# Performance work log

Measured on AMD Instinct MI355X. Metric: run time of the kernel, lower is better.

Reference implementation:

```python
import jax, jax.numpy as jnp
import numpy as np

B, N, H, NB, NCT = 8, 4096, 1024, 128, 33
LN_EPS = 1e-5


def setup_inputs() -> dict:
    key = jax.random.key(0)
    ks = jax.random.split(key, 12)
    x = jax.random.normal(ks[0], (B, N, H), dtype=jnp.float32)
    cancer_type = jax.random.randint(ks[1], (B,), 0, NCT)
    block_ids = jax.random.randint(ks[2], (B, N), 0, NB)
    pad_mask = jnp.zeros((B, N), dtype=bool)
    s1 = 1.0 / np.sqrt(H)
    s2 = 1.0 / np.sqrt(H // 2)
    return {
        "x": x,
        "cancer_type": cancer_type,
        "block_ids": block_ids,
        "pad_mask": pad_mask,
        "W1": jax.random.normal(ks[3], (H, H // 2), jnp.float32) * s1,
        "b1": jnp.zeros((H // 2,), jnp.float32),
        "W2": jax.random.normal(ks[4], (H // 2, 1), jnp.float32) * s2,
        "b2": jnp.zeros((1,), jnp.float32),
        "ct_emb": jax.random.normal(ks[5], (NCT, NB), jnp.float32) * 0.1,
        "Wp": jax.random.normal(ks[6], (H, H), jnp.float32) * s1,
        "bp": jnp.zeros((H,), jnp.float32),
        "ln_g": jnp.ones((H,), jnp.float32),
        "ln_b": jnp.zeros((H,), jnp.float32),
    }


def reference(x, cancer_type, block_ids, pad_mask, W1, b1, W2, b2, ct_emb, Wp, bp, ln_g, ln_b):
    nb = ct_emb.shape[1]
    # gate MLP: (B,N)
    h = jnp.tanh(x @ W1 + b1)
    gate = (h @ W2 + b2)[..., 0]
    valid = ~pad_mask
    # block membership mask (B, NB, N)
    mask = (block_ids[:, None, :] == jnp.arange(nb)[None, :, None]) & valid[:, None, :]
    neg_inf = jnp.float32(-jnp.inf)
    scores = jnp.where(mask, gate[:, None, :], neg_inf)
    # stable masked softmax over N; empty blocks -> all-zero weights (nan_to_num(0))
    m = jnp.max(scores, axis=-1, keepdims=True)
    m = jnp.where(jnp.isfinite(m), m, 0.0)
    e = jnp.where(mask, jnp.exp(scores - m), 0.0)
    denom = jnp.sum(e, axis=-1, keepdims=True)
    w = jnp.where(denom > 0, e / jnp.maximum(denom, 1e-30), 0.0)
    # cancer-type modulation: weights * (1 + 0.1*ct_mod[:,bid])
    ct_mod = ct_emb[cancer_type]  # (B, NB)
    w = w * (1.0 + 0.1 * ct_mod)[:, :, None]
    # pooled per-block token (B, NB, H)
    pooled = jnp.einsum('bkn,bnh->bkh', w, x)
    # block_proj: Linear -> LayerNorm -> ELU (dropout = eval identity)
    y = pooled @ Wp + bp
    mu = jnp.mean(y, axis=-1, keepdims=True)
    var = jnp.mean((y - mu) ** 2, axis=-1, keepdims=True)
    y = (y - mu) * jax.lax.rsqrt(var + LN_EPS) * ln_g + ln_b
    y = jax.nn.elu(y)
    has_b = jnp.any(mask, axis=-1)              # (B, NB)
    present = jnp.any(has_b, axis=0)            # (NB,) torch loop skips blocks absent everywhere
    block_tokens = jnp.where(present[None, :, None], y, 0.0)
    return block_tokens, has_b
```

## Files before the change

### kernel.cpp

```cpp
#include <hip/hip_runtime.h>

#define NTOK 4096
#define HDIM 1024
#define HHALF 512
#define NBLK 128
#define CAP 256
#define XELEMS 33554432ull

typedef __attribute__((ext_vector_type(8))) short short8;
typedef __attribute__((ext_vector_type(4))) float f32x4;
typedef short bf16s;

__device__ __forceinline__ short f2bf(float f) {
    unsigned u = __builtin_bit_cast(unsigned, f);
    u = (u + 0x7fffu + ((u >> 16) & 1u)) >> 16;
    return (short)u;
}
__device__ __forceinline__ void gload_lds16(const void* g, void* l) {
    __builtin_amdgcn_global_load_lds(
        (const __attribute__((address_space(1))) unsigned int*)g,
        (__attribute__((address_space(3))) unsigned int*)l, 16, 0, 0);
}
__device__ __forceinline__ float fast_tanh(float v) {
    float e = __expf(2.0f * v);
    return 1.0f - 2.0f / (e + 1.0f);
}

__global__ void k_xcvt(const float* __restrict__ in, bf16s* __restrict__ out) {
    for (size_t i = ((size_t)blockIdx.x * 256 + threadIdx.x) * 8; i < XELEMS;
         i += (size_t)gridDim.x * 256 * 8) {
        float4 a = *reinterpret_cast<const float4*>(&in[i]);
        float4 b = *reinterpret_cast<const float4*>(&in[i + 4]);
        short h[8] = {f2bf(a.x), f2bf(a.y), f2bf(a.z), f2bf(a.w),
                      f2bf(b.x), f2bf(b.y), f2bf(b.z), f2bf(b.w)};
        *reinterpret_cast<int4*>(&out[i]) = *reinterpret_cast<const int4*>(h);
    }
}

__global__ void k_tcvt2(const float* __restrict__ W1, const float* __restrict__ Wp,
                        bf16s* __restrict__ w1t, bf16s* __restrict__ wpt) {
    __shared__ float tile[64][65];
    const int by = blockIdx.y;
    const float* in = (by < 8) ? W1 : Wp;
    bf16s* out = (by < 8) ? w1t : wpt;
    const int Nc = (by < 8) ? HHALF : HDIM;
    const int n0 = ((by < 8) ? by : (by - 8)) * 64;
    const int k0 = blockIdx.x * 64;
    const int tx = threadIdx.x & 63, ty = threadIdx.x >> 6;
    #pragma unroll
    for (int i = 0; i < 16; ++i) {
        int r = ty + i * 4;
        tile[r][tx] = in[(size_t)(k0 + r) * Nc + n0 + tx];
    }
    __syncthreads();
    #pragma unroll
    for (int i = 0; i < 16; ++i) {
        int r = ty + i * 4;
        out[(size_t)(n0 + r) * 1024 + k0 + tx] = f2bf(tile[tx][r]);
    }
}

__global__ __launch_bounds__(512, 1) void k_gemm8(
    const bf16s* __restrict__ xb, const bf16s* __restrict__ w1t,
    const float* __restrict__ b1, const float* __restrict__ w2,
    float* __restrict__ partial)
{
    __shared__ alignas(16) bf16s As[2][256 * 32];
    __shared__ alignas(16) bf16s Bs[2][256 * 32];

    const int tid = threadIdx.x;
    const int lane = tid & 63;
    const int wv = tid >> 6;
    const int wm = wv >> 2;
    const int wn = wv & 3;
    const int phys = blockIdx.x;
    const int logical = (phys & 7) * 32 + (phys >> 3);
    const int row0 = (logical >> 1) * 256;
    const int ct   = logical & 1;
    const int col0 = ct * 256;
    const int c0 = lane & 15, khalf = lane >> 4;

    const int sj = (lane & 3) ^ ((lane >> 3) & 3);
    const int rA0 = ((wv & 4) ? 128 : 0) + (wv & 3) * 16 + (lane >> 2);
    const int rB0 = wv * 16 + (lane >> 2);
    const bf16s* aS0 = &xb [(size_t)(row0 + rA0) * HDIM + sj * 8];
    const bf16s* aS1 = aS0 + (size_t)64 * HDIM;
    const bf16s* bS0 = &w1t[(size_t)(col0 + rB0) * HDIM + sj * 8];
    const bf16s* bS1 = bS0 + (size_t)128 * HDIM;
    const int adst0 = (((wv & 4) ? 128 : 0) + (wv & 3) * 16) * 32 + lane * 8;
    const int adst1 = adst0 + 64 * 32;
    const int bdst0 = (wv * 16) * 32 + lane * 8;
    const int bdst1 = bdst0 + 128 * 32;

    const int ch8 = (khalf ^ ((c0 >> 1) & 3)) * 8;
    const int arA = (wm * 128 + c0) * 32 + ch8;
    const int brB = (wn * 64 + c0) * 32 + ch8;

    f32x4 acc[8][4] = {};
    short8 bvv[4];
    short8 av[4];

#define MFMA16(MB)                                                            \
    __builtin_amdgcn_s_setprio(1);                                           \
    _Pragma("unroll")                                                         \
    for (int n = 0; n < 4; ++n)                                               \
        _Pragma("unroll")                                                     \
        for (int m = 0; m < 4; ++m)                                           \
            acc[(MB) + m][n] =                                                \
                __builtin_amdgcn_mfma_f32_16x16x32_bf16(av[m], bvv[n],        \
                                                        acc[(MB) + m][n], 0, 0, 0); \
    __builtin_amdgcn_s_setprio(0);

    gload_lds16(aS0, &As[0][adst0]);
    gload_lds16(aS1, &As[0][adst1]);
    gload_lds16(bS0, &Bs[0][bdst0]);
    gload_lds16(bS1, &Bs[0][bdst1]);
    gload_lds16(aS0 + 32, &As[1][adst0]);
    gload_lds16(bS0 + 32, &Bs[1][bdst0]);

    for (int it = 0; it < 16; ++it) {
        const int ka = 2 * it, kb = 2 * it + 1;
        const bool nl = (it < 15);

        gload_lds16(aS1 + kb * 32, &As[1][adst1]);
        gload_lds16(bS1 + kb * 32, &Bs[1][bdst1]);
        asm volatile("s_waitcnt vmcnt(4)" ::: "memory");
        __builtin_amdgcn_s_barrier();
        #pragma unroll
        for (int m = 0; m < 4; ++m)
            av[m] = *reinterpret_cast<const short8*>(&As[0][arA + m * 512]);
        #pragma unroll
        for (int n = 0; n < 4; ++n)
            bvv[n] = *reinterpret_cast<const short8*>(&Bs[0][brB + n * 512]);
        asm volatile("s_waitcnt lgkmcnt(0)" ::: "memory");
        __builtin_amdgcn_sched_barrier(0);
        MFMA16(0)
        __builtin_amdgcn_s_barrier();

        #pragma unroll
        for (int m = 0; m < 4; ++m)
            av[m] = *reinterpret_cast<const short8*>(&As[0][arA + (4 + m) * 512]);
        if (nl) {
            gload_lds16(aS0 + (ka + 2) * 32, &As[0][adst0]);
            gload_lds16(bS0 + (ka + 2) * 32, &Bs[0][bdst0]);
        }
        __builtin_amdgcn_s_barrier();
        asm volatile("s_waitcnt lgkmcnt(0)" ::: "memory");
        __builtin_amdgcn_sched_barrier(0);
        MFMA16(4)
        __builtin_amdgcn_s_barrier();

        if (nl) {
            gload_lds16(aS1 + (ka + 2) * 32, &As[0][adst1]);
            gload_lds16(bS1 + (ka + 2) * 32, &Bs[0][bdst1]);
            asm volatile("s_waitcnt vmcnt(4)" ::: "memory");
        } else {
            asm volatile("s_waitcnt vmcnt(0)" ::: "memory");
        }
        __builtin_amdgcn_s_barrier();
        #pragma unroll
        for (int m = 0; m < 4; ++m)
            av[m] = *reinterpret_cast<const short8*>(&As[1][arA + m * 512]);
        #pragma unroll
        for (int n = 0; n < 4; ++n)
            bvv[n] = *reinterpret_cast<const short8*>(&Bs[1][brB + n * 512]);
        asm volatile("s_waitcnt lgkmcnt(0)" ::: "memory");
        __builtin_amdgcn_sched_barrier(0);
        MFMA16(0)
        __builtin_amdgcn_s_barrier();

        #pragma unroll
        for (int m = 0; m < 4; ++m)
            av[m] = *reinterpret_cast<const short8*>(&As[1][arA + (4 + m) * 512]);
        if (nl) {
            gload_lds16(aS0 + (kb + 2) * 32, &As[1][adst0]);
            gload_lds16(bS0 + (kb + 2) * 32, &Bs[1][bdst0]);
        }
        __builtin_amdgcn_s_barrier();
        asm volatile("s_waitcnt lgkmcnt(0)" ::: "memory");
        __builtin_amdgcn_sched_barrier(0);
        MFMA16(4)
        __builtin_amdgcn_s_barrier();
    }
#undef MFMA16

    float* gp = reinterpret_cast<float*>(&As[0][0]);
    float b1v[4], w2v[4];
    #pragma unroll
    for (int nf = 0; nf < 4; ++nf) {
        int gc = col0 + wn * 64 + nf * 16 + c0;
        b1v[nf] = b1[gc];
        w2v[nf] = w2[gc];
    }
    #pragma unroll
    for (int mf = 0; mf < 8; ++mf) {
        #pragma unroll
        for (int reg = 0; reg < 4; ++reg) {
            float s = 0.f;
            #pragma unroll
            for (int nf = 0; nf < 4; ++nf)
                s += fast_tanh(acc[mf][nf][reg] + b1v[nf]) * w2v[nf];
            s += __shfl_xor(s, 1); s += __shfl_xor(s, 2);
            s += __shfl_xor(s, 4); s += __shfl_xor(s, 8);
            if (c0 == 0)
                gp[wn * 256 + wm * 128 + mf * 16 + khalf * 4 + reg] = s;
        }
    }
    __syncthreads();
    if (tid < 256)
        partial[(size_t)ct * 32768 + row0 + tid] =
            gp[tid] + gp[256 + tid] + gp[512 + tid] + gp[768 + tid];
}

__global__ void k_blocks(const int* __restrict__ block_ids, const unsigned char* __restrict__ pad,
                         const float* __restrict__ part, const float* __restrict__ b2,
                         float* __restrict__ gate, const int* __restrict__ ct,
                         const float* __restrict__ ct_emb,
                         int* __restrict__ counts, float* __restrict__ mblk,
                         float* __restrict__ wscale, int* __restrict__ lists,
                         float* __restrict__ out_hasb)
{
    const int blk = blockIdx.x;
    const int b = blk >> 7, k = blk & 127;
    const int lane = threadIdx.x;
    const int base = b * NTOK;
    const int lbase = blk * CAP;
    const unsigned long long ltmask = (1ull << lane) - 1ull;
    const float b2v = b2[0];

    float m = -__builtin_inff();
    float s = 0.f;
    int pos = 0;
    for (int t0 = 0; t0 < NTOK; t0 += 64) {
        int t = t0 + lane;
        bool mt = (block_ids[base + t] == k) && (pad[base + t] == 0);
        unsigned long long mask = __ballot(mt);
        if (mt) {
            int r = base + t;
            float g = part[r] + part[32768 + r] + b2v;
            gate[r] = g;
            int my = pos + __popcll(mask & ltmask);
            if (my < CAP) lists[lbase + my] = t;
            float mn = fmaxf(m, g);
            s = s * __expf(m - mn) + __expf(g - mn);
            m = mn;
        }
        pos += __popcll(mask);
    }
    #pragma unroll
    for (int off = 1; off < 64; off <<= 1) {
        float om = __shfl_xor(m, off);
        float os = __shfl_xor(s, off);
        float mn = fmaxf(m, om);
        float sa = (m == -__builtin_inff()) ? 0.f : s * __expf(m - mn);
        float sb = (om == -__builtin_inff()) ? 0.f : os * __expf(om - mn);
        s = sa + sb;
        m = mn;
    }
    if (lane == 0) {
        counts[blk] = pos;
        mblk[blk] = (pos > 0) ? m : 0.f;
        float mod = 1.0f + 0.1f * ct_emb[ct[b] * NBLK + k];
        wscale[blk] = (pos > 0 && s > 0.f) ? (mod / fmaxf(s, 1e-30f)) : 0.f;
        out_hasb[blk] = (pos > 0) ? 1.f : 0.f;
    }
}

__global__ void k_pool(const bf16s* __restrict__ xb, const float* __restrict__ gate,
                       const int* __restrict__ lists, const int* __restrict__ counts,
                       const float* __restrict__ mblk, const float* __restrict__ wscale,
                       bf16s* __restrict__ pooled)
{
    const int blk = blockIdx.x;
    const int b = blk >> 7;
    const int tid = threadIdx.x;
    const int base = b * NTOK;
    const int cnt = min(counts[blk], CAP);
    const int lbase = blk * CAP;
    const float m = mblk[blk], ws = wscale[blk];

    float4 acc = {0.f, 0.f, 0.f, 0.f};
    for (int i = 0; i < cnt; ++i) {
        int n = lists[lbase + i];
        float w = __expf(gate[base + n] - m);
        int2 rv = *reinterpret_cast<const int2*>(&xb[(size_t)(base + n) * HDIM + tid * 4]);
        short s4[4];
        *reinterpret_cast<int2*>(s4) = rv;
        unsigned u0 = ((unsigned)(unsigned short)s4[0]) << 16;
        unsigned u1 = ((unsigned)(unsigned short)s4[1]) << 16;
        unsigned u2 = ((unsigned)(unsigned short)s4[2]) << 16;
        unsigned u3 = ((unsigned)(unsigned short)s4[3]) << 16;
        acc.x += w * __builtin_bit_cast(float, u0);
        acc.y += w * __builtin_bit_cast(float, u1);
        acc.z += w * __builtin_bit_cast(float, u2);
        acc.w += w * __builtin_bit_cast(float, u3);
    }
    short o[4] = {f2bf(acc.x * ws), f2bf(acc.y * ws), f2bf(acc.z * ws), f2bf(acc.w * ws)};
    *reinterpret_cast<int2*>(&pooled[(size_t)blk * HDIM + tid * 4]) =
        *reinterpret_cast<const int2*>(o);
}

__global__ __launch_bounds__(256) void k_gemm2(
    const bf16s* __restrict__ pooled, const bf16s* __restrict__ wpt,
    const float* __restrict__ bp, float* __restrict__ y)
{
    __shared__ alignas(16) bf16s As[2][64 * 32];
    __shared__ alignas(16) bf16s Bs[2][64 * 32];
    const int tid = threadIdx.x;
    const int lane = tid & 63;
    const int wv = tid >> 6;
    const int wr = wv >> 1, wc = wv & 1;
    const int row0 = (blockIdx.x >> 4) * 64, col0 = (blockIdx.x & 15) * 64;
    const int c0 = lane & 15, khalf = lane >> 4;

    const int sr = wv * 16 + (lane >> 2);
    const int sj = (lane & 3) ^ ((sr >> 1) & 3);
    const int sdst = (wv * 16) * 32 + lane * 8;
    const bf16s* srcA = &pooled[(size_t)(row0 + sr) * 1024 + sj * 8];
    const bf16s* srcB = &wpt[(size_t)(col0 + sr) * 1024 + sj * 8];

    f32x4 acc[2][2] = {};

    gload_lds16(srcA, &As[0][sdst]);
    gload_lds16(srcB, &Bs[0][sdst]);

    for (int t = 0; t < 32; ++t) {
        const int cur = t & 1;
        if (t < 31) {
            gload_lds16(srcA + (t + 1) * 32, &As[cur ^ 1][sdst]);
            gload_lds16(srcB + (t + 1) * 32, &Bs[cur ^ 1][sdst]);
            asm volatile("s_waitcnt vmcnt(2)" ::: "memory");
        } else {
            asm volatile("s_waitcnt vmcnt(0)" ::: "memory");
        }
        __builtin_amdgcn_s_barrier();
        __builtin_amdgcn_sched_barrier(0);
        #pragma unroll
        for (int mf = 0; mf < 2; ++mf) {
            int ra = wr * 32 + mf * 16 + c0;
            short8 av = *reinterpret_cast<const short8*>(
                &As[cur][ra * 32 + ((khalf ^ ((ra >> 1) & 3)) * 8)]);
            #pragma unroll
            for (int nf = 0; nf < 2; ++nf) {
                int rb = wc * 32 + nf * 16 + c0;
                short8 bv = *reinterpret_cast<const short8*>(
                    &Bs[cur][rb * 32 + ((khalf ^ ((rb >> 1) & 3)) * 8)]);
                acc[mf][nf] = __builtin_amdgcn_mfma_f32_16x16x32_bf16(av, bv, acc[mf][nf], 0, 0, 0);
            }
        }
        asm volatile("s_waitcnt lgkmcnt(0)" ::: "memory");
        __builtin_amdgcn_sched_barrier(0);
        __builtin_amdgcn_s_barrier();
    }
    #pragma unroll
    for (int mf = 0; mf < 2; ++mf)
        #pragma unroll
        for (int nf = 0; nf < 2; ++nf)
            #pragma unroll
            for (int reg = 0; reg < 4; ++reg) {
                int grow = row0 + wr * 32 + mf * 16 + khalf * 4 + reg;
                int gcol = col0 + wc * 32 + nf * 16 + c0;
                y[(size_t)grow * 1024 + gcol] = acc[mf][nf][reg] + bp[gcol];
            }
}

__global__ void k_lnelu(const float* __restrict__ y, const float* __restrict__ ln_g,
                        const float* __restrict__ ln_b, const int* __restrict__ counts,
                        float* __restrict__ outp)
{
    const int row = blockIdx.x;
    const int k = row & 127;
    const int tid = threadIdx.x;

    float4 v = *reinterpret_cast<const float4*>(&y[(size_t)row * 1024 + tid * 4]);
    float s = v.x + v.y + v.z + v.w;
    float ss = v.x * v.x + v.y * v.y + v.z * v.z + v.w * v.w;
    #pragma unroll
    for (int off = 32; off; off >>= 1) { s += __shfl_xor(s, off); ss += __shfl_xor(ss, off); }

    __shared__ float sbuf[4], ssbuf[4];
    int wv = tid >> 6;
    if ((tid & 63) == 0) { sbuf[wv] = s; ssbuf[wv] = ss; }
    __syncthreads();
    s = sbuf[0] + sbuf[1] + sbuf[2] + sbuf[3];
    ss = ssbuf[0] + ssbuf[1] + ssbuf[2] + ssbuf[3];

    float mu = s * (1.f / 1024.f);
    float var = ss * (1.f / 1024.f) - mu * mu;
    float rstd = rsqrtf(var + 1e-5f);

    bool pres = false;
    #pragma unroll
    for (int bb = 0; bb < 8; ++bb) pres = pres || (counts[bb * NBLK + k] > 0);

    float4 g4 = *reinterpret_cast<const float4*>(&ln_g[tid * 4]);
    float4 b4 = *reinterpret_cast<const float4*>(&ln_b[tid * 4]);
    float vals[4] = {v.x, v.y, v.z, v.w};
    float gs[4] = {g4.x, g4.y, g4.z, g4.w};
    float bs[4] = {b4.x, b4.y, b4.z, b4.w};
    float4 o;
    float* op = &o.x;
    #pragma unroll
    for (int j = 0; j < 4; ++j) {
        float t = (vals[j] - mu) * rstd * gs[j] + bs[j];
        t = (t > 0.f) ? t : expm1f(t);
        op[j] = pres ? t : 0.f;
    }
    *reinterpret_cast<float4*>(&outp[(size_t)row * 1024 + tid * 4]) = o;
}

extern "C" void kernel_launch(void* const* d_in, const int* in_sizes, int n_in,
                              void* d_out, int out_size, void* d_ws, size_t ws_size,
                              hipStream_t stream)
{
    const float* x      = (const float*)d_in[0];
    const int*   ct     = (const int*)d_in[1];
    const int*   bids   = (const int*)d_in[2];
    const unsigned char* pad = (const unsigned char*)d_in[3];
    const float* W1     = (const float*)d_in[4];
    const float* b1     = (const float*)d_in[5];
    const float* W2     = (const float*)d_in[6];
    const float* b2     = (const float*)d_in[7];
    const float* ct_emb = (const float*)d_in[8];
    const float* Wp     = (const float*)d_in[9];
    const float* bp     = (const float*)d_in[10];
    const float* ln_g   = (const float*)d_in[11];
    const float* ln_b   = (const float*)d_in[12];
    float* outF = (float*)d_out;

    char* ws = (char*)d_ws;
    bf16s* w1t    = (bf16s*)(ws + 0);
    bf16s* wpt    = (bf16s*)(ws + 1048576);
    float* gate   = (float*)(ws + 3145728);
    float* part   = (float*)(ws + 3276800);
    float* mblk   = (float*)(ws + 3801088);
    float* wscal  = (float*)(ws + 3805184);
    int*   counts = (int*)  (ws + 3809280);
    int*   lists  = (int*)  (ws + 3813376);
    bf16s* pooled = (bf16s*)(ws + 4861952);
    float* ybuf   = (float*)(ws + 6959104);
    bf16s* xb     = (bf16s*)(ws + 11153408);

    k_tcvt2<<<dim3(16, 24), 256, 0, stream>>>(W1, Wp, w1t, wpt);
    k_xcvt<<<2048, 256, 0, stream>>>(x, xb);
    k_gemm8<<<256, 512, 0, stream>>>(xb, w1t, b1, W2, part);
    k_blocks<<<1024, 64, 0, stream>>>(bids, pad, part, b2, gate, ct, ct_emb,
                                      counts, mblk, wscal, lists,
                                      outF + (size_t)8 * NBLK * HDIM);
    k_pool<<<1024, 256, 0, stream>>>(xb, gate, lists, counts, mblk, wscal, pooled);
    k_gemm2<<<256, 256, 0, stream>>>(pooled, wpt, bp, ybuf);
    k_lnelu<<<1024, 256, 0, stream>>>(ybuf, ln_g, ln_b, counts, outF);
}
```

Before: 144.3 us.

## Fuse fp32-to-bf16 conversion of x into gate GEMM and pool from fp32

Removes the standalone pass that converts the whole activation tensor to bf16. The gate GEMM now loads fp32 rows into registers, converts them and writes bf16 into shared memory, with a register prefetch one k-step ahead. The pooling kernel reads fp32 x directly. This cuts a full read/write pass and a kernel launch, but the GEMM loses direct global-to-LDS loads for A and gains register pressure and conversion work in its main loop.

```diff
diff --git a/kernel.cpp b/kernel.cpp
--- a/kernel.cpp
+++ b/kernel.cpp
@@ -5,7 +5,6 @@
 #define HHALF 512
 #define NBLK 128
 #define CAP 256
-#define XELEMS 33554432ull
 
 typedef __attribute__((ext_vector_type(8))) short short8;
 typedef __attribute__((ext_vector_type(4))) float f32x4;
@@ -24,17 +23,6 @@
 __device__ __forceinline__ float fast_tanh(float v) {
     float e = __expf(2.0f * v);
     return 1.0f - 2.0f / (e + 1.0f);
-}
-
-__global__ void k_xcvt(const float* __restrict__ in, bf16s* __restrict__ out) {
-    for (size_t i = ((size_t)blockIdx.x * 256 + threadIdx.x) * 8; i < XELEMS;
-         i += (size_t)gridDim.x * 256 * 8) {
-        float4 a = *reinterpret_cast<const float4*>(&in[i]);
-        float4 b = *reinterpret_cast<const float4*>(&in[i + 4]);
-        short h[8] = {f2bf(a.x), f2bf(a.y), f2bf(a.z), f2bf(a.w),
-                      f2bf(b.x), f2bf(b.y), f2bf(b.z), f2bf(b.w)};
-        *reinterpret_cast<int4*>(&out[i]) = *reinterpret_cast<const int4*>(h);
-    }
 }
 
 __global__ void k_tcvt2(const float* __restrict__ W1, const float* __restrict__ Wp,
@@ -60,8 +48,8 @@
     }
 }
 
-__global__ __launch_bounds__(512, 1) void k_gemm8(
-    const bf16s* __restrict__ xb, const bf16s* __restrict__ w1t,
+__global__ __launch_bounds__(512, 1) void k_gemm8f(
+    const float* __restrict__ x, const bf16s* __restrict__ w1t,
     const float* __restrict__ b1, const float* __restrict__ w2,
     float* __restrict__ partial)
 {
@@ -76,19 +64,19 @@
     const int phys = blockIdx.x;
     const int logical = (phys & 7) * 32 + (phys >> 3);
     const int row0 = (logical >> 1) * 256;
-    const int ct   = logical & 1;
-    const int col0 = ct * 256;
+    const int ctile = logical & 1;
+    const int col0 = ctile * 256;
     const int c0 = lane & 15, khalf = lane >> 4;
 
     const int sj = (lane & 3) ^ ((lane >> 3) & 3);
-    const int rA0 = ((wv & 4) ? 128 : 0) + (wv & 3) * 16 + (lane >> 2);
-    const int rB0 = wv * 16 + (lane >> 2);
-    const bf16s* aS0 = &xb [(size_t)(row0 + rA0) * HDIM + sj * 8];
-    const bf16s* aS1 = aS0 + (size_t)64 * HDIM;
-    const bf16s* bS0 = &w1t[(size_t)(col0 + rB0) * HDIM + sj * 8];
-    const bf16s* bS1 = bS0 + (size_t)128 * HDIM;
+    const int arow0 = ((wv & 4) ? 128 : 0) + (wv & 3) * 16 + (lane >> 2);
+    const float* aF0 = &x[(size_t)(row0 + arow0) * HDIM + sj * 8];
+    const float* aF1 = aF0 + (size_t)64 * HDIM;
     const int adst0 = (((wv & 4) ? 128 : 0) + (wv & 3) * 16) * 32 + lane * 8;
     const int adst1 = adst0 + 64 * 32;
+    const int brow0 = wv * 16 + (lane >> 2);
+    const bf16s* bS0 = &w1t[(size_t)(col0 + brow0) * HDIM + sj * 8];
+    const bf16s* bS1 = bS0 + (size_t)128 * HDIM;
     const int bdst0 = (wv * 16) * 32 + lane * 8;
     const int bdst1 = bdst0 + 128 * 32;
 
@@ -97,8 +85,7 @@
     const int brB = (wn * 64 + c0) * 32 + ch8;
 
     f32x4 acc[8][4] = {};
-    short8 bvv[4];
-    short8 av[4];
+    short8 av[4], bvv[4];
 
 #define MFMA16(MB)                                                            \
     __builtin_amdgcn_s_setprio(1);                                           \
@@ -111,19 +98,33 @@
                                                         acc[(MB) + m][n], 0, 0, 0); \
     __builtin_amdgcn_s_setprio(0);
 
-    gload_lds16(aS0, &As[0][adst0]);
-    gload_lds16(aS1, &As[0][adst1]);
+#define CVTWR(U0, U1, DST, BUF) do {                                          \
+        short h_[8] = {f2bf((U0).x), f2bf((U0).y), f2bf((U0).z), f2bf((U0).w),\
+                       f2bf((U1).x), f2bf((U1).y), f2bf((U1).z), f2bf((U1).w)};\
+        *reinterpret_cast<int4*>(&As[BUF][DST]) =                             \
+            *reinterpret_cast<const int4*>(h_);                               \
+    } while (0)
+
+    {
+        float4 p0 = *reinterpret_cast<const float4*>(aF0);
+        float4 p1 = *reinterpret_cast<const float4*>(aF0 + 4);
+        float4 p2 = *reinterpret_cast<const float4*>(aF1);
+        float4 p3 = *reinterpret_cast<const float4*>(aF1 + 4);
+        CVTWR(p0, p1, adst0, 0);
+        CVTWR(p2, p3, adst1, 0);
+    }
     gload_lds16(bS0, &Bs[0][bdst0]);
     gload_lds16(bS1, &Bs[0][bdst1]);
-    gload_lds16(aS0 + 32, &As[1][adst0]);
-    gload_lds16(bS0 + 32, &Bs[1][bdst0]);
+    float4 ra0 = *reinterpret_cast<const float4*>(aF0 + 32);
+    float4 ra1 = *reinterpret_cast<const float4*>(aF0 + 36);
+    float4 ra2 = *reinterpret_cast<const float4*>(aF1 + 32);
+    float4 ra3 = *reinterpret_cast<const float4*>(aF1 + 36);
+    float4 rb0, rb1, rb2, rb3;
+    asm volatile("s_waitcnt lgkmcnt(0)" ::: "memory");
 
     for (int it = 0; it < 16; ++it) {
-        const int ka = 2 * it, kb = 2 * it + 1;
-        const bool nl = (it < 15);
-
-        gload_lds16(aS1 + kb * 32, &As[1][adst1]);
-        gload_lds16(bS1 + kb * 32, &Bs[1][bdst1]);
+        const int ka = 2 * it, kb = ka + 1;
+
         asm volatile("s_waitcnt vmcnt(4)" ::: "memory");
         __builtin_amdgcn_s_barrier();
         #pragma unroll
@@ -132,27 +133,31 @@
         #pragma unroll
         for (int n = 0; n < 4; ++n)
             bvv[n] = *reinterpret_cast<const short8*>(&Bs[0][brB + n * 512]);
+        CVTWR(ra0, ra1, adst0, 1);
+        gload_lds16(bS0 + (ka + 1) * 32, &Bs[1][bdst0]);
         asm volatile("s_waitcnt lgkmcnt(0)" ::: "memory");
         __builtin_amdgcn_sched_barrier(0);
         MFMA16(0)
         __builtin_amdgcn_s_barrier();
-
         #pragma unroll
         for (int m = 0; m < 4; ++m)
             av[m] = *reinterpret_cast<const short8*>(&As[0][arA + (4 + m) * 512]);
+        CVTWR(ra2, ra3, adst1, 1);
+        gload_lds16(bS1 + (ka + 1) * 32, &Bs[1][bdst1]);
+        if (ka < 30) {
+            rb0 = *reinterpret_cast<const float4*>(aF0 + (ka + 2) * 32);
+            rb1 = *reinterpret_cast<const float4*>(aF0 + (ka + 2) * 32 + 4);
+            rb2 = *reinterpret_cast<const float4*>(aF1 + (ka + 2) * 32);
+            rb3 = *reinterpret_cast<const float4*>(aF1 + (ka + 2) * 32 + 4);
+        }
+        __builtin_amdgcn_s_barrier();
+        asm volatile("s_waitcnt lgkmcnt(0)" ::: "memory");
+        __builtin_amdgcn_sched_barrier(0);
+        MFMA16(4)
+        __builtin_amdgcn_s_barrier();
+
+        const bool nl = (kb < 31);
         if (nl) {
-            gload_lds16(aS0 + (ka + 2) * 32, &As[0][adst0]);
-            gload_lds16(bS0 + (ka + 2) * 32, &Bs[0][bdst0]);
-        }
-        __builtin_amdgcn_s_barrier();
-        asm volatile("s_waitcnt lgkmcnt(0)" ::: "memory");
-        __builtin_amdgcn_sched_barrier(0);
-        MFMA16(4)
-        __builtin_amdgcn_s_barrier();
-
-        if (nl) {
-            gload_lds16(aS1 + (ka + 2) * 32, &As[0][adst1]);
-            gload_lds16(bS1 + (ka + 2) * 32, &Bs[0][bdst1]);
             asm volatile("s_waitcnt vmcnt(4)" ::: "memory");
         } else {
             asm volatile("s_waitcnt vmcnt(0)" ::: "memory");
@@ -164,17 +169,26 @@
         #pragma unroll
         for (int n = 0; n < 4; ++n)
             bvv[n] = *reinterpret_cast<const short8*>(&Bs[1][brB + n * 512]);
+        if (nl) {
+            CVTWR(rb0, rb1, adst0, 0);
+            gload_lds16(bS0 + (kb + 1) * 32, &Bs[0][bdst0]);
+        }
         asm volatile("s_waitcnt lgkmcnt(0)" ::: "memory");
         __builtin_amdgcn_sched_barrier(0);
         MFMA16(0)
         __builtin_amdgcn_s_barrier();
-
         #pragma unroll
         for (int m = 0; m < 4; ++m)
             av[m] = *reinterpret_cast<const short8*>(&As[1][arA + (4 + m) * 512]);
         if (nl) {
-            gload_lds16(aS0 + (kb + 2) * 32, &As[1][adst0]);
-            gload_lds16(bS0 + (kb + 2) * 32, &Bs[1][bdst0]);
+            CVTWR(rb2, rb3, adst1, 0);
+            gload_lds16(bS1 + (kb + 1) * 32, &Bs[0][bdst1]);
+        }
+        if (kb < 30) {
+            ra0 = *reinterpret_cast<const float4*>(aF0 + (kb + 2) * 32);
+            ra1 = *reinterpret_cast<const float4*>(aF0 + (kb + 2) * 32 + 4);
+            ra2 = *reinterpret_cast<const float4*>(aF1 + (kb + 2) * 32);
+            ra3 = *reinterpret_cast<const float4*>(aF1 + (kb + 2) * 32 + 4);
         }
         __builtin_amdgcn_s_barrier();
         asm volatile("s_waitcnt lgkmcnt(0)" ::: "memory");
@@ -183,6 +197,7 @@
         __builtin_amdgcn_s_barrier();
     }
 #undef MFMA16
+#undef CVTWR
 
     float* gp = reinterpret_cast<float*>(&As[0][0]);
     float b1v[4], w2v[4];
@@ -208,7 +223,7 @@
     }
     __syncthreads();
     if (tid < 256)
-        partial[(size_t)ct * 32768 + row0 + tid] =
+        partial[(size_t)ctile * 32768 + row0 + tid] =
             gp[tid] + gp[256 + tid] + gp[512 + tid] + gp[768 + tid];
 }
 
@@ -266,7 +281,7 @@
     }
 }
 
-__global__ void k_pool(const bf16s* __restrict__ xb, const float* __restrict__ gate,
+__global__ void k_pool(const float* __restrict__ x, const float* __restrict__ gate,
                        const int* __restrict__ lists, const int* __restrict__ counts,
                        const float* __restrict__ mblk, const float* __restrict__ wscale,
                        bf16s* __restrict__ pooled)
@@ -283,17 +298,8 @@
     for (int i = 0; i < cnt; ++i) {
         int n = lists[lbase + i];
         float w = __expf(gate[base + n] - m);
-        int2 rv = *reinterpret_cast<const int2*>(&xb[(size_t)(base + n) * HDIM + tid * 4]);
-        short s4[4];
-        *reinterpret_cast<int2*>(s4) = rv;
-        unsigned u0 = ((unsigned)(unsigned short)s4[0]) << 16;
-        unsigned u1 = ((unsigned)(unsigned short)s4[1]) << 16;
-        unsigned u2 = ((unsigned)(unsigned short)s4[2]) << 16;
-        unsigned u3 = ((unsigned)(unsigned short)s4[3]) << 16;
-        acc.x += w * __builtin_bit_cast(float, u0);
-        acc.y += w * __builtin_bit_cast(float, u1);
-        acc.z += w * __builtin_bit_cast(float, u2);
-        acc.w += w * __builtin_bit_cast(float, u3);
+        float4 xv = *reinterpret_cast<const float4*>(&x[(size_t)(base + n) * HDIM + tid * 4]);
+        acc.x += w * xv.x; acc.y += w * xv.y; acc.z += w * xv.z; acc.w += w * xv.w;
     }
     short o[4] = {f2bf(acc.x * ws), f2bf(acc.y * ws), f2bf(acc.z * ws), f2bf(acc.w * ws)};
     *reinterpret_cast<int2*>(&pooled[(size_t)blk * HDIM + tid * 4]) =
@@ -439,15 +445,13 @@
     int*   lists  = (int*)  (ws + 3813376);
     bf16s* pooled = (bf16s*)(ws + 4861952);
     float* ybuf   = (float*)(ws + 6959104);
-    bf16s* xb     = (bf16s*)(ws + 11153408);
 
     k_tcvt2<<<dim3(16, 24), 256, 0, stream>>>(W1, Wp, w1t, wpt);
-    k_xcvt<<<2048, 256, 0, stream>>>(x, xb);
-    k_gemm8<<<256, 512, 0, stream>>>(xb, w1t, b1, W2, part);
+    k_gemm8f<<<256, 512, 0, stream>>>(x, w1t, b1, W2, part);
     k_blocks<<<1024, 64, 0, stream>>>(bids, pad, part, b2, gate, ct, ct_emb,
                                       counts, mblk, wscal, lists,
                                       outF + (size_t)8 * NBLK * HDIM);
-    k_pool<<<1024, 256, 0, stream>>>(xb, gate, lists, counts, mblk, wscal, pooled);
+    k_pool<<<1024, 256, 0, stream>>>(x, gate, lists, counts, mblk, wscal, pooled);
     k_gemm2<<<256, 256, 0, stream>>>(pooled, wpt, bp, ybuf);
     k_lnelu<<<1024, 256, 0, stream>>>(ybuf, ln_g, ln_b, counts, outF);
 }
```

Result: faster. 129.1 us (-10.5%).
